# Optimization experiments

Hardware: AMD Instinct MI355X
Metric: run time of the kernel (lower is better)

## Reference

```python
import jax, jax.numpy as jnp
import numpy as np

N_X = 20000      # bessel x-grid
N_ELL = 48       # sparse tabulated multipoles
N_K = 1024       # k quadrature points
N_TAU = 600      # conformal-time samples
K_PIVOT = 0.05


def fast_interp(x, xmin, xmax, ytab):
    """Uniform-grid linear interpolation (tools.fast_interp). ytab: [Nx]."""
    n = ytab.shape[0]
    pos = jnp.clip((x - xmin) / (xmax - xmin) * (n - 1), 0.0, n - 1.0)
    i0 = jnp.clip(jnp.floor(pos).astype(jnp.int32), 0, n - 2)
    w = pos - i0
    return ytab[i0] * (1.0 - w) + ytab[i0 + 1] * w


def setup_inputs() -> dict:
    key = jax.random.key(0)
    ks = jax.random.split(key, 8)
    k = jnp.logspace(-4.0, 0.0, N_K, dtype=jnp.float32)           # Mpc^-1
    tau = jnp.linspace(50.0, 14000.0, N_TAU, dtype=jnp.float32)    # Mpc
    tau0 = jnp.asarray(14100.0, dtype=jnp.float32)
    bessel_x_tab = jnp.linspace(0.0, 15000.0, N_X, dtype=jnp.float32)
    mk = lambda kk, sh, s: (s * jax.random.normal(kk, sh, dtype=jnp.float32))
    return {
        "k": k,
        "tau": tau,
        "tau0": tau0,
        "S0": mk(ks[0], (N_K, N_TAU), 1e-2),
        "S1": mk(ks[1], (N_K, N_TAU), 1e-2),
        "S2": mk(ks[2], (N_K, N_TAU), 1e-2),
        "SE": mk(ks[3], (N_K, N_TAU), 1e-2),
        "bessel_x_tab": bessel_x_tab,
        "phi0_tab": mk(ks[4], (N_X, N_ELL), 1e-1),
        "phi1_tab": mk(ks[5], (N_X, N_ELL), 1e-1),
        "phi2_tab": mk(ks[6], (N_X, N_ELL), 1e-1),
        "eps_tab": mk(ks[7], (N_X, N_ELL), 1e-1),
        "A_s": jnp.asarray(2.1e-9, dtype=jnp.float32),
        "n_s": jnp.asarray(0.965, dtype=jnp.float32),
    }


def reference(k, tau, tau0, S0, S1, S2, SE, bessel_x_tab,
              phi0_tab, phi1_tab, phi2_tab, eps_tab, A_s, n_s):
    xmin = bessel_x_tab[0]
    xmax = bessel_x_tab[-1]
    # radial argument x = k * (tau0 - tau): [K, T]
    x = k[:, None] * (tau0 - tau)[None, :]

    def one_ell(p0, p1, p2, pe):
        # lookup phi0/phi1/phi2/epsilon at every (k, tau), fuse with sources
        srcT = (S0 * fast_interp(x, xmin, xmax, p0)
                + S1 * fast_interp(x, xmin, xmax, p1)
                + S2 * fast_interp(x, xmin, xmax, p2))
        Tl = jnp.trapezoid(srcT, tau, axis=-1)                       # [K]
        El = jnp.trapezoid(SE * fast_interp(x, xmin, xmax, pe), tau, axis=-1)
        return Tl, El

    # vmap over the tabulated-ell axis (columns of the Bessel tables)
    Tl, El = jax.vmap(one_ell, in_axes=(1, 1, 1, 1))(
        phi0_tab, phi1_tab, phi2_tab, eps_tab)                       # [L, K]

    # primordial curvature spectrum P_R(k) = A_s (k/k_p)^(n_s-1) * 2 pi^2 / k^3
    P_R = A_s * (k / K_PIVOT) ** (n_s - 1.0) * (2.0 * jnp.pi ** 2 / k ** 3)
    w = k * k * P_R                                                   # [K]
    c = 2.0 / jnp.pi
    ClTT = c * jnp.trapezoid(w * Tl * Tl, k, axis=-1)                 # [L]
    ClEE = c * jnp.trapezoid(w * El * El, k, axis=-1)
    ClTE = c * jnp.trapezoid(w * Tl * El, k, axis=-1)
    return jnp.stack([ClTT, ClEE, ClTE], axis=0)                      # [3, L]
```

## Files before the change

### kernel.cpp

```cpp
#include <hip/hip_runtime.h>
#include <math.h>

#define N_X   20000
#define N_ELL 48
#define N_K   1024
#define N_TAU 600
#define SPLIT 8
#define CHUNK (N_TAU / SPLIT)

__device__ __forceinline__ unsigned int pack_half2(float lo, float hi) {
    _Float16 l = (_Float16)lo, h = (_Float16)hi;
    unsigned short lu = __builtin_bit_cast(unsigned short, l);
    unsigned short hu = __builtin_bit_cast(unsigned short, h);
    return (unsigned int)lu | ((unsigned int)hu << 16);
}
__device__ __forceinline__ float fdot2(unsigned int a, unsigned int b, float c) {
    float d;
    asm("v_dot2_f32_f16 %0, %1, %2, %3" : "=v"(d) : "v"(a), "v"(b), "v"(c));
    return d;
}

__global__ __launch_bounds__(256) void repack_kernel(
    const float* __restrict__ p0, const float* __restrict__ p1,
    const float* __restrict__ p2, const float* __restrict__ pe,
    uint4* __restrict__ P)
{
    const int total = N_X * N_ELL;
    for (int idx = blockIdx.x * blockDim.x + threadIdx.x; idx < total;
         idx += gridDim.x * blockDim.x) {
        int x = idx / N_ELL;
        int e = idx - x * N_ELL;
        int xn = (x < N_X - 1) ? x + 1 : x;
        int a = x * N_ELL + e, b = xn * N_ELL + e;
        uint4 v;
        v.x = pack_half2(p0[a], p0[b]);
        v.y = pack_half2(p1[a], p1[b]);
        v.z = pack_half2(p2[a], p2[b]);
        v.w = pack_half2(pe[a], pe[b]);
        P[idx] = v;
    }
}

__global__ __launch_bounds__(256, 8) void tl_el_packed(
    const float* __restrict__ k, const float* __restrict__ tau,
    const float* __restrict__ tau0p,
    const float* __restrict__ S0, const float* __restrict__ S1,
    const float* __restrict__ S2, const float* __restrict__ SE,
    const float* __restrict__ bx, const uint4* __restrict__ P,
    float* __restrict__ Tlp, float* __restrict__ Elp)
{
    const int bid  = blockIdx.x;
    const int part = bid & (SPLIT - 1);
    const int kgrp = bid >> 3;
    const int tid  = threadIdx.x;
    const int wave = tid >> 6;
    const int lane = tid & 63;
    const int ell  = (lane < N_ELL) ? lane : (N_ELL - 1);
    const int kidx = (N_K - 1) - (4 * kgrp + wave);
    const int t0   = part * CHUNK;

    __shared__ unsigned int off_s[4][CHUNK];
    __shared__ uint4        W2_s[4][CHUNK];

    const float kk    = k[kidx];
    const float tau0  = tau0p[0];
    const float xmin  = bx[0];
    const float xmax  = bx[N_X - 1];
    const float scale = (float)(N_X - 1) / (xmax - xmin);

    for (int tl = lane; tl < CHUNK; tl += 64) {
        int t = t0 + tl;
        float tt = tau[t];
        float tp = (t > 0)         ? tau[t - 1] : tt;
        float tn = (t < N_TAU - 1) ? tau[t + 1] : tt;
        float wt = 0.5f * (tn - tp);
        float x   = kk * (tau0 - tt);
        float pos = (x - xmin) * scale;
        pos = fminf(fmaxf(pos, 0.0f), (float)(N_X - 1));
        int i0 = (int)pos;
        if (i0 > N_X - 2) i0 = N_X - 2;
        float w  = pos - (float)i0;
        float om = 1.0f - w;
        size_t sb = (size_t)kidx * N_TAU + t;
        float s0 = wt * S0[sb], s1 = wt * S1[sb];
        float s2 = wt * S2[sb], se = wt * SE[sb];
        uint4 w2;
        w2.x = pack_half2(s0 * om, s0 * w);
        w2.y = pack_half2(s1 * om, s1 * w);
        w2.z = pack_half2(s2 * om, s2 * w);
        w2.w = pack_half2(se * om, se * w);
        W2_s[wave][tl]  = w2;
        off_s[wave][tl] = (unsigned int)i0 * (N_ELL * 16u);
    }
    __syncthreads();

    const char* Pb = (const char*)P;
    const unsigned int elloff = (unsigned int)ell * 16u;
    float aT0 = 0.0f, aT1 = 0.0f, aT2 = 0.0f, aE = 0.0f;

    #pragma unroll 3
    for (int i = 0; i < CHUNK; ++i) {
        unsigned int voff = off_s[wave][i] + elloff;
        uint4 pr = *(const uint4*)(Pb + voff);
        uint4 w2 = W2_s[wave][i];
        aT0 = fdot2(pr.x, w2.x, aT0);
        aT1 = fdot2(pr.y, w2.y, aT1);
        aT2 = fdot2(pr.z, w2.z, aT2);
        aE  = fdot2(pr.w, w2.w, aE);
    }
    float accT = (aT0 + aT1) + aT2;

    if (lane < N_ELL) {
        Tlp[((size_t)part * N_ELL + lane) * N_K + kidx] = accT;
        Elp[((size_t)part * N_ELL + lane) * N_K + kidx] = aE;
    }
}

__global__ __launch_bounds__(256) void tl_el_kernel(
    const float* __restrict__ k, const float* __restrict__ tau,
    const float* __restrict__ tau0p,
    const float* __restrict__ S0, const float* __restrict__ S1,
    const float* __restrict__ S2, const float* __restrict__ SE,
    const float* __restrict__ bx,
    const float* __restrict__ p0, const float* __restrict__ p1,
    const float* __restrict__ p2, const float* __restrict__ pe,
    float* __restrict__ Tl, float* __restrict__ El)
{
    const int kidx = blockIdx.x;
    const int tid  = threadIdx.x;
    const int wave = tid >> 6;
    const int lane = tid & 63;
    const int ell  = (lane < N_ELL) ? lane : (N_ELL - 1);

    const float kk    = k[kidx];
    const float tau0  = tau0p[0];
    const float xmin  = bx[0];
    const float xmax  = bx[N_X - 1];
    const float scale = (float)(N_X - 1) / (xmax - xmin);

    const float* Srow0 = S0 + (size_t)kidx * N_TAU;
    const float* Srow1 = S1 + (size_t)kidx * N_TAU;
    const float* Srow2 = S2 + (size_t)kidx * N_TAU;
    const float* SrowE = SE + (size_t)kidx * N_TAU;

    float accT = 0.0f, accE = 0.0f;

    for (int t = wave; t < N_TAU; t += 4) {
        float tt    = tau[t];
        float tprev = (t > 0)         ? tau[t - 1] : tt;
        float tnext = (t < N_TAU - 1) ? tau[t + 1] : tt;
        float wt    = 0.5f * (tnext - tprev);

        float x   = kk * (tau0 - tt);
        float pos = (x - xmin) * scale;
        pos = fminf(fmaxf(pos, 0.0f), (float)(N_X - 1));
        int i0 = (int)floorf(pos);
        if (i0 > N_X - 2) i0 = N_X - 2;
        float w = pos - (float)i0;

        int base = i0 * N_ELL + ell;
        float y00 = p0[base], y01 = p0[base + N_ELL];
        float y10 = p1[base], y11 = p1[base + N_ELL];
        float y20 = p2[base], y21 = p2[base + N_ELL];
        float ye0 = pe[base], ye1 = pe[base + N_ELL];

        float a0 = fmaf(w, y01 - y00, y00);
        float a1 = fmaf(w, y11 - y10, y10);
        float a2 = fmaf(w, y21 - y20, y20);
        float ae = fmaf(w, ye1 - ye0, ye0);

        float s0 = Srow0[t], s1 = Srow1[t], s2 = Srow2[t], se = SrowE[t];

        float srcT = s0 * a0 + s1 * a1 + s2 * a2;
        accT = fmaf(wt, srcT, accT);
        accE = fmaf(wt, se * ae, accE);
    }

    __shared__ float redT[4][N_ELL];
    __shared__ float redE[4][N_ELL];
    if (lane < N_ELL) { redT[wave][lane] = accT; redE[wave][lane] = accE; }
    __syncthreads();
    if (tid < N_ELL) {
        float sT = (redT[0][tid] + redT[1][tid]) + (redT[2][tid] + redT[3][tid]);
        float sE = (redE[0][tid] + redE[1][tid]) + (redE[2][tid] + redE[3][tid]);
        Tl[tid * N_K + kidx] = sT;
        El[tid * N_K + kidx] = sE;
    }
}

__global__ __launch_bounds__(256) void cl_kernel(
    const float* __restrict__ k,
    const float* __restrict__ Asp, const float* __restrict__ nsp,
    const float* __restrict__ Tlp, const float* __restrict__ Elp,
    int nparts, float* __restrict__ out)
{
    const int ell = blockIdx.x;
    const int tid = threadIdx.x;
    const float A_s = Asp[0];
    const float n_s = nsp[0];
    const float two_pi2 = 2.0f * (float)M_PI * (float)M_PI;

    float aTT = 0.0f, aEE = 0.0f, aTE = 0.0f;
    for (int i = tid; i < N_K; i += 256) {
        float kv    = k[i];
        float kprev = (i > 0)       ? k[i - 1] : kv;
        float knext = (i < N_K - 1) ? k[i + 1] : kv;
        float dkw   = 0.5f * (knext - kprev);
        float Pw = A_s * powf(kv / 0.05f, n_s - 1.0f) * two_pi2 / kv;
        float ww = dkw * Pw;
        float tl = 0.0f, el = 0.0f;
        for (int p = 0; p < nparts; ++p) {
            tl += Tlp[((size_t)p * N_ELL + ell) * N_K + i];
            el += Elp[((size_t)p * N_ELL + ell) * N_K + i];
        }
        aTT = fmaf(ww * tl, tl, aTT);
        aEE = fmaf(ww * el, el, aEE);
        aTE = fmaf(ww * tl, el, aTE);
    }

    for (int off = 32; off > 0; off >>= 1) {
        aTT += __shfl_down(aTT, off, 64);
        aEE += __shfl_down(aEE, off, 64);
        aTE += __shfl_down(aTE, off, 64);
    }
    __shared__ float red[3][4];
    const int wave = tid >> 6, lane = tid & 63;
    if (lane == 0) { red[0][wave] = aTT; red[1][wave] = aEE; red[2][wave] = aTE; }
    __syncthreads();
    if (tid == 0) {
        const float c = 2.0f / (float)M_PI;
        out[0 * N_ELL + ell] = c * ((red[0][0] + red[0][1]) + (red[0][2] + red[0][3]));
        out[1 * N_ELL + ell] = c * ((red[1][0] + red[1][1]) + (red[1][2] + red[1][3]));
        out[2 * N_ELL + ell] = c * ((red[2][0] + red[2][1]) + (red[2][2] + red[2][3]));
    }
}

extern "C" void kernel_launch(void* const* d_in, const int* in_sizes, int n_in,
                              void* d_out, int out_size, void* d_ws, size_t ws_size,
                              hipStream_t stream) {
    const float* k    = (const float*)d_in[0];
    const float* tau  = (const float*)d_in[1];
    const float* tau0 = (const float*)d_in[2];
    const float* S0   = (const float*)d_in[3];
    const float* S1   = (const float*)d_in[4];
    const float* S2   = (const float*)d_in[5];
    const float* SE   = (const float*)d_in[6];
    const float* bx   = (const float*)d_in[7];
    const float* p0   = (const float*)d_in[8];
    const float* p1   = (const float*)d_in[9];
    const float* p2   = (const float*)d_in[10];
    const float* pe   = (const float*)d_in[11];
    const float* A_s  = (const float*)d_in[12];
    const float* n_s  = (const float*)d_in[13];
    float* out = (float*)d_out;

    const size_t P_bytes    = (size_t)N_X * N_ELL * sizeof(uint4);
    const size_t part_bytes = (size_t)SPLIT * N_ELL * N_K * sizeof(float);

    if (ws_size >= P_bytes + 2 * part_bytes) {
        uint4* P   = (uint4*)d_ws;
        float* Tlp = (float*)((char*)d_ws + P_bytes);
        float* Elp = (float*)((char*)d_ws + P_bytes + part_bytes);

        repack_kernel<<<(N_X * N_ELL + 255) / 256, 256, 0, stream>>>(p0, p1, p2, pe, P);
        tl_el_packed<<<(N_K / 4) * SPLIT, 256, 0, stream>>>(k, tau, tau0,
                                                            S0, S1, S2, SE, bx,
                                                            P, Tlp, Elp);
        cl_kernel<<<N_ELL, 256, 0, stream>>>(k, A_s, n_s, Tlp, Elp, SPLIT, out);
    } else {
        float* Tl = (float*)d_ws;
        float* El = Tl + (size_t)N_ELL * N_K;
        tl_el_kernel<<<N_K, 256, 0, stream>>>(k, tau, tau0, S0, S1, S2, SE, bx,
                                              p0, p1, p2, pe, Tl, El);
        cl_kernel<<<N_ELL, 256, 0, stream>>>(k, A_s, n_s, Tl, El, 1, out);
    }
}
```

Baseline: 136.1 us.

## Halve packed Bessel table by dropping duplicated neighbor entries

```diff
diff --git a/kernel.cpp b/kernel.cpp
--- a/kernel.cpp
+++ b/kernel.cpp
@@ -19,24 +19,20 @@
     asm("v_dot2_f32_f16 %0, %1, %2, %3" : "=v"(d) : "v"(a), "v"(b), "v"(c));
     return d;
 }
+#define SEL_LO 0x05040100u
+#define SEL_HI 0x07060302u
 
 __global__ __launch_bounds__(256) void repack_kernel(
     const float* __restrict__ p0, const float* __restrict__ p1,
     const float* __restrict__ p2, const float* __restrict__ pe,
-    uint4* __restrict__ P)
+    uint2* __restrict__ P)
 {
     const int total = N_X * N_ELL;
     for (int idx = blockIdx.x * blockDim.x + threadIdx.x; idx < total;
          idx += gridDim.x * blockDim.x) {
-        int x = idx / N_ELL;
-        int e = idx - x * N_ELL;
-        int xn = (x < N_X - 1) ? x + 1 : x;
-        int a = x * N_ELL + e, b = xn * N_ELL + e;
-        uint4 v;
-        v.x = pack_half2(p0[a], p0[b]);
-        v.y = pack_half2(p1[a], p1[b]);
-        v.z = pack_half2(p2[a], p2[b]);
-        v.w = pack_half2(pe[a], pe[b]);
+        uint2 v;
+        v.x = pack_half2(p0[idx], p1[idx]);
+        v.y = pack_half2(p2[idx], pe[idx]);
         P[idx] = v;
     }
 }
@@ -46,7 +42,7 @@
     const float* __restrict__ tau0p,
     const float* __restrict__ S0, const float* __restrict__ S1,
     const float* __restrict__ S2, const float* __restrict__ SE,
-    const float* __restrict__ bx, const uint4* __restrict__ P,
+    const float* __restrict__ bx, const uint2* __restrict__ P,
     float* __restrict__ Tlp, float* __restrict__ Elp)
 {
     const int bid  = blockIdx.x;
@@ -90,23 +86,31 @@
         w2.z = pack_half2(s2 * om, s2 * w);
         w2.w = pack_half2(se * om, se * w);
         W2_s[wave][tl]  = w2;
-        off_s[wave][tl] = (unsigned int)i0 * (N_ELL * 16u);
+        off_s[wave][tl] = (unsigned int)i0 * (N_ELL * 8u);
     }
     __syncthreads();
 
     const char* Pb = (const char*)P;
-    const unsigned int elloff = (unsigned int)ell * 16u;
+    const unsigned int elloff = (unsigned int)ell * 8u;
     float aT0 = 0.0f, aT1 = 0.0f, aT2 = 0.0f, aE = 0.0f;
 
-    #pragma unroll 3
+    #pragma unroll 5
     for (int i = 0; i < CHUNK; ++i) {
         unsigned int voff = off_s[wave][i] + elloff;
-        uint4 pr = *(const uint4*)(Pb + voff);
+        const uint2* rp = (const uint2*)(Pb + voff);
+        uint2 ra = rp[0];
+        uint2 rb = rp[N_ELL];
         uint4 w2 = W2_s[wave][i];
-        aT0 = fdot2(pr.x, w2.x, aT0);
-        aT1 = fdot2(pr.y, w2.y, aT1);
-        aT2 = fdot2(pr.z, w2.z, aT2);
-        aE  = fdot2(pr.w, w2.w, aE);
+
+        unsigned int pr0 = __builtin_amdgcn_perm(rb.x, ra.x, SEL_LO);
+        unsigned int pr1 = __builtin_amdgcn_perm(rb.x, ra.x, SEL_HI);
+        unsigned int pr2 = __builtin_amdgcn_perm(rb.y, ra.y, SEL_LO);
+        unsigned int pre = __builtin_amdgcn_perm(rb.y, ra.y, SEL_HI);
+
+        aT0 = fdot2(pr0, w2.x, aT0);
+        aT1 = fdot2(pr1, w2.y, aT1);
+        aT2 = fdot2(pr2, w2.z, aT2);
+        aE  = fdot2(pre, w2.w, aE);
     }
     float accT = (aT0 + aT1) + aT2;
 
@@ -254,11 +258,11 @@
     const float* n_s  = (const float*)d_in[13];
     float* out = (float*)d_out;
 
-    const size_t P_bytes    = (size_t)N_X * N_ELL * sizeof(uint4);
+    const size_t P_bytes    = (size_t)N_X * N_ELL * sizeof(uint2);
     const size_t part_bytes = (size_t)SPLIT * N_ELL * N_K * sizeof(float);
 
     if (ws_size >= P_bytes + 2 * part_bytes) {
-        uint4* P   = (uint4*)d_ws;
+        uint2* P   = (uint2*)d_ws;
         float* Tlp = (float*)((char*)d_ws + P_bytes);
         float* Elp = (float*)((char*)d_ws + P_bytes + part_bytes);
 
```

Result: slower. 149.6 us (+9.9%).
